# Kernel optimization log

Measured on AMD Instinct MI355X. Metric: run time of the kernel, lower is better.

Reference implementation:

```python
import jax, jax.numpy as jnp
import numpy as np

N, E, D, B, C = 50000, 800000, 128, 20000, 40
EPS_BN = 1e-3    # keras BatchNormalization default epsilon
EPS_NRM = 1e-12  # keras ops.nn.normalize epsilon
FFN_DIMS = {"pre": (D, D), "c1p": (D, D), "c1u": (2 * D, D), "c2p": (D, D), "c2u": (2 * D, D), "post": (D, D)}


def setup_inputs() -> dict:
    key = jax.random.key(0)
    ks = jax.random.split(key, 8)
    inp = {
        "node_features": jax.random.normal(ks[0], (N, D), jnp.float32),
        "edges": jax.random.randint(ks[1], (2, E), 0, N, dtype=jnp.int32),
        "edge_w": jax.random.uniform(ks[2], (E,), jnp.float32),
        "input_node_idx": jax.random.randint(ks[3], (B,), 0, N, dtype=jnp.int32),
    }
    for i, (name, (din, dout)) in enumerate(FFN_DIMS.items()):
        kw = jax.random.fold_in(key, 100 + i)
        inp[name + "_g"] = jnp.ones((din,), jnp.float32)
        inp[name + "_be"] = jnp.zeros((din,), jnp.float32)
        inp[name + "_mu"] = jnp.zeros((din,), jnp.float32)
        inp[name + "_var"] = jnp.ones((din,), jnp.float32)
        inp[name + "_w"] = jax.random.normal(kw, (din, dout), jnp.float32) * (1.0 / float(np.sqrt(din)))
        inp[name + "_bi"] = jnp.zeros((dout,), jnp.float32)
    inp["logits_w"] = jax.random.normal(ks[4], (D, C), jnp.float32) * (1.0 / float(np.sqrt(D)))
    inp["logits_b"] = jnp.zeros((C,), jnp.float32)
    return inp


def ffn(x, g, be, mu, var, w, bi):
    # BatchNorm (inference running stats) -> Dropout (identity) -> Dense + exact gelu
    xn = (x - mu) * jax.lax.rsqrt(var + EPS_BN) * g + be
    return jax.nn.gelu(xn @ w + bi, approximate=False)


def l2norm(x):
    n = jnp.sqrt(jnp.sum(x * x, axis=-1, keepdims=True))
    return x / jnp.maximum(n, EPS_NRM)


def graph_conv(x, node_idx, nbr_idx, ew, prep, upd):
    # gather neighbours -> prepare FFN -> edge-weighted -> segment_sum (reduce='sum')
    msgs = ffn(x[nbr_idx], *prep) * ew[:, None]                         # [E, D]
    red = jax.ops.segment_sum(msgs, node_idx, num_segments=x.shape[0])  # [N, D]
    h = jnp.concatenate([x, red], axis=1)                               # [N, 2D] (combination='concat')
    return l2norm(ffn(h, *upd))                                         # normalize=True


def reference(node_features, edges, edge_w, input_node_idx,
              pre_g, pre_be, pre_mu, pre_var, pre_w, pre_bi,
              c1p_g, c1p_be, c1p_mu, c1p_var, c1p_w, c1p_bi,
              c1u_g, c1u_be, c1u_mu, c1u_var, c1u_w, c1u_bi,
              c2p_g, c2p_be, c2p_mu, c2p_var, c2p_w, c2p_bi,
              c2u_g, c2u_be, c2u_mu, c2u_var, c2u_w, c2u_bi,
              post_g, post_be, post_mu, post_var, post_w, post_bi,
              logits_w, logits_b):
    ew = edge_w / jnp.sum(edge_w)                       # edge_W normalized at init
    node_idx, nbr_idx = edges[0], edges[1]
    x = ffn(node_features, pre_g, pre_be, pre_mu, pre_var, pre_w, pre_bi)
    x = graph_conv(x, node_idx, nbr_idx, ew,
                   (c1p_g, c1p_be, c1p_mu, c1p_var, c1p_w, c1p_bi),
                   (c1u_g, c1u_be, c1u_mu, c1u_var, c1u_w, c1u_bi)) + x
    x = graph_conv(x, node_idx, nbr_idx, ew,
                   (c2p_g, c2p_be, c2p_mu, c2p_var, c2p_w, c2p_bi),
                   (c2u_g, c2u_be, c2u_mu, c2u_var, c2u_w, c2u_bi)) + x
    x = ffn(x, post_g, post_be, post_mu, post_var, post_w, post_bi)
    return x[input_node_idx] @ logits_w + logits_b      # [B, C]
```

## Files before the change

kernel.cpp:

```cpp
#include <hip/hip_runtime.h>
#include <hip/hip_fp16.h>
#include <math.h>

static constexpr int D = 128;
static constexpr int CAP = 64;
static constexpr float EPS_BN = 1e-3f;

typedef short short8 __attribute__((ext_vector_type(8)));
typedef short short4v __attribute__((ext_vector_type(4)));
typedef float float4v __attribute__((ext_vector_type(4)));

__device__ __forceinline__ float gelu_exact(float x) {
    return 0.5f * x * (1.0f + erff(x * 0.70710678118654752f));
}

__device__ __forceinline__ void f32_to_hilo(float f, short& h, short& l) {
    unsigned u = __float_as_uint(f);
    h = (short)(u >> 16);
    float hf = __uint_as_float(u & 0xFFFF0000u);
    unsigned lu = __float_as_uint(f - hf);
    l = (short)(lu >> 16);
}

__device__ __forceinline__ short f32_to_bf16_rne(float f) {
    unsigned u = __float_as_uint(f);
    u += 0x7FFFu + ((u >> 16) & 1u);
    return (short)(u >> 16);
}

__device__ __forceinline__ void cvt_hilo8(const float4& x, const float4& y, short8& h8, short8& l8) {
    short h, l;
    f32_to_hilo(x.x, h, l); h8[0] = h; l8[0] = l;
    f32_to_hilo(x.y, h, l); h8[1] = h; l8[1] = l;
    f32_to_hilo(x.z, h, l); h8[2] = h; l8[2] = l;
    f32_to_hilo(x.w, h, l); h8[3] = h; l8[3] = l;
    f32_to_hilo(y.x, h, l); h8[4] = h; l8[4] = l;
    f32_to_hilo(y.y, h, l); h8[5] = h; l8[5] = l;
    f32_to_hilo(y.z, h, l); h8[6] = h; l8[6] = l;
    f32_to_hilo(y.w, h, l); h8[7] = h; l8[7] = l;
}

__device__ __forceinline__ short8 cvt_rne8(const float4& x, const float4& y) {
    short8 r;
    r[0] = f32_to_bf16_rne(x.x); r[1] = f32_to_bf16_rne(x.y);
    r[2] = f32_to_bf16_rne(x.z); r[3] = f32_to_bf16_rne(x.w);
    r[4] = f32_to_bf16_rne(y.x); r[5] = f32_to_bf16_rne(y.y);
    r[6] = f32_to_bf16_rne(y.z); r[7] = f32_to_bf16_rne(y.w);
    return r;
}

struct FoldArgs {
    const float* g[6]; const float* be[6]; const float* mu[6];
    const float* var[6]; const float* w[6]; const float* bi[6];
    short* wh[6]; short* wl[6]; float* bp[6]; int K[6];
};

__global__ void k_fold(FoldArgs fa) {
    __shared__ float sm[4];
    const int tid = threadIdx.x;
    const int lane = tid & 63, wvi = tid >> 6;
    const int f = blockIdx.x >> 7;
    const int c = blockIdx.x & 127;
    const int K = fa.K[f];
    const float* g = fa.g[f]; const float* be = fa.be[f];
    const float* mu = fa.mu[f]; const float* var = fa.var[f];
    const float* w = fa.w[f]; const float* bi = fa.bi[f];
    short* wh = fa.wh[f]; short* wl = fa.wl[f]; float* bp = fa.bp[f];
    float part = 0.f;
    for (int k = tid; k < K; k += blockDim.x) {
        float a = g[k] / sqrtf(var[k] + EPS_BN);
        float wv = w[k * D + c];
        float prod = a * wv;
        short hh, ll;
        f32_to_hilo(prod, hh, ll);
        wh[c * K + k] = hh;
        wl[c * K + k] = ll;
        part += (be[k] - mu[k] * a) * wv;
    }
    for (int off = 32; off > 0; off >>= 1) part += __shfl_down(part, off, 64);
    if (lane == 0) sm[wvi] = part;
    __syncthreads();
    if (tid == 0) bp[c] = bi[c] + sm[0] + sm[1] + sm[2] + sm[3];
}

__global__ void __launch_bounds__(512) k_fillpre(
    const int* __restrict__ edges, const float* __restrict__ ew,
    int* __restrict__ cnt, float* __restrict__ sums, unsigned* __restrict__ cw,
    int E, int N,
    const float* __restrict__ A0, const short* __restrict__ Wh,
    const short* __restrict__ Wl, const float* __restrict__ bp,
    float* __restrict__ outf,
    const short* __restrict__ Wh1, const float* __restrict__ bp1,
    __half* __restrict__ yh)
{
    constexpr int K = 128;
    constexpr int WSZ = 128 * K;
    __shared__ short Wlds[2 * WSZ];
    __shared__ short xbuf[2][16][136];
    __shared__ float sm[8];

    const int tid = threadIdx.x;
    const int lane = tid & 63;
    const int wvi = tid >> 6;

    if ((int)blockIdx.x < 256) {
        const int rid = blockIdx.x;
        const int g = rid & 7;
        const int bid = rid >> 3;
        const int gstride = 32 * 512;
        const int N8 = (N + 7) >> 3;
        const int lo = g * N8;
        const int hi = min(lo + N8, N);
        float s = 0.f;
        for (int e = bid * 512 + tid; e < E; e += gstride) {
            int dst = edges[e];
            if (dst >= lo && dst < hi) {
                int src = edges[E + e];
                float w = ew[e];
                s += w;
                unsigned short wb = __half_as_ushort(__float2half(w));
                int idx = atomicAdd(&cnt[dst], 1);
                if (idx < CAP)
                    cw[(size_t)dst * CAP + idx] = ((unsigned)src << 16) | (unsigned)wb;
            }
        }
        for (int off = 32; off > 0; off >>= 1) s += __shfl_down(s, off, 64);
        if (lane == 0) sm[wvi] = s;
        __syncthreads();
        if (tid == 0) {
            float t = 0.f;
            #pragma unroll
            for (int i = 0; i < 8; i++) t += sm[i];
            if (t != 0.f) atomicAdd(sums, t);
        }
        return;
    }

    const int fbid = blockIdx.x - 256;
    constexpr int NBLK = 768;

    #pragma unroll
    for (int it = 0; it < (2 * WSZ) / (512 * 8); ++it) {
        int s = it * 4096 + tid * 8;
        int buf = s / WSZ;
        int rem = s - buf * WSZ;
        int c = rem / K;
        int kk = (rem & (K - 1)) ^ ((c & 7) << 3);
        const short* src = (buf ? Wl : Wh) + c * K + kk;
        *(short8*)&Wlds[s] = *(const short8*)src;
    }
    __syncthreads();

    const int wv = tid >> 6;
    const int ssub = wv >> 2;
    const int wc = wv & 3;
    const int m = lane & 15;
    const int quad = lane >> 4;
    const int nstrips = (N + 15) >> 4;
    constexpr int STRIDE = NBLK * 2;

    int remw = nstrips - fbid * 2;
    int nit = remw > 0 ? (remw + STRIDE - 1) / STRIDE : 0;

    for (int it = 0; it < nit; ++it) {
        const int strip = fbid * 2 + ssub + it * STRIDE;
        const bool active = strip < nstrips;
        float4v acc[2];
        acc[0] = (float4v){0.f, 0.f, 0.f, 0.f};
        acc[1] = (float4v){0.f, 0.f, 0.f, 0.f};

        if (active) {
            int r = strip * 16 + m;
            if (r >= N) r = N - 1;
            const float* pA0 = A0 + (size_t)r * D;

            float4 a[2][4];
            {
                const float4* s4 = (const float4*)pA0 + quad * 2;
                a[0][0] = s4[0]; a[0][1] = s4[1]; a[0][2] = s4[8]; a[0][3] = s4[9];
            }
            {
                const float4* s4 = (const float4*)(pA0 + 64) + quad * 2;
                a[1][0] = s4[0]; a[1][1] = s4[1]; a[1][2] = s4[8]; a[1][3] = s4[9];
            }

            #pragma unroll
            for (int cc = 0; cc < 2; ++cc) {
                #pragma unroll
                for (int ks = 0; ks < 2; ++ks) {
                    const int kk = cc * 64 + ks * 32 + quad * 8;
                    short8 ah, al;
                    cvt_hilo8(a[cc][ks * 2], a[cc][ks * 2 + 1], ah, al);
                    #pragma unroll
                    for (int tj = 0; tj < 2; ++tj) {
                        const int c = wc * 32 + tj * 16 + m;
                        const int idx = c * K + (kk ^ ((c & 7) << 3));
                        short8 bh = *(const short8*)&Wlds[idx];
                        short8 bl = *(const short8*)&Wlds[WSZ + idx];
                        acc[tj] = __builtin_amdgcn_mfma_f32_16x16x32_bf16(al, bh, acc[tj], 0, 0, 0);
                        acc[tj] = __builtin_amdgcn_mfma_f32_16x16x32_bf16(ah, bl, acc[tj], 0, 0, 0);
                        acc[tj] = __builtin_amdgcn_mfma_f32_16x16x32_bf16(ah, bh, acc[tj], 0, 0, 0);
                    }
                }
            }

            #pragma unroll
            for (int tj = 0; tj < 2; ++tj) {
                float bv = bp[wc * 32 + tj * 16 + m];
                #pragma unroll
                for (int r4 = 0; r4 < 4; ++r4)
                    acc[tj][r4] = gelu_exact(acc[tj][r4] + bv);
            }
            #pragma unroll
            for (int r4 = 0; r4 < 4; ++r4) {
                int rib = quad * 4 + r4;
                int row = strip * 16 + rib;
                #pragma unroll
                for (int tj = 0; tj < 2; ++tj) {
                    int col = wc * 32 + tj * 16 + m;
                    if (row < N) outf[(size_t)row * D + col] = acc[tj][r4];
                    xbuf[ssub][rib][col] = f32_to_bf16_rne(acc[tj][r4]);
                }
            }
        }
        __syncthreads();

        if (active) {
            float4v acc2[2];
            acc2[0] = (float4v){0.f, 0.f, 0.f, 0.f};
            acc2[1] = (float4v){0.f, 0.f, 0.f, 0.f};
            #pragma unroll
            for (int cc = 0; cc < 2; ++cc) {
                #pragma unroll
                for (int ks = 0; ks < 2; ++ks) {
                    const int kk = cc * 64 + ks * 32 + quad * 8;
                    short8 ah = *(const short8*)&xbuf[ssub][m][kk];
                    #pragma unroll
                    for (int tj = 0; tj < 2; ++tj) {
                        const int c = wc * 32 + tj * 16 + m;
                        short8 bh = *(const short8*)(Wh1 + (size_t)c * 128 + kk);
                        acc2[tj] = __builtin_amdgcn_mfma_f32_16x16x32_bf16(ah, bh, acc2[tj], 0, 0, 0);
                    }
                }
            }
            #pragma unroll
            for (int tj = 0; tj < 2; ++tj) {
                float bv = bp1[wc * 32 + tj * 16 + m];
                #pragma unroll
                for (int r4 = 0; r4 < 4; ++r4)
                    acc2[tj][r4] = gelu_exact(acc2[tj][r4] + bv);
            }
            #pragma unroll
            for (int r4 = 0; r4 < 4; ++r4) {
                int row = strip * 16 + quad * 4 + r4;
                if (row < N) {
                    #pragma unroll
                    for (int tj = 0; tj < 2; ++tj) {
                        int col = wc * 32 + tj * 16 + m;
                        yh[(size_t)row * D + col] = __float2half(acc2[tj][r4]);
                    }
                }
            }
        }
        __syncthreads();
    }
}

__device__ __forceinline__ void accum8(float* acc, const float4& raw, float w) {
    const __half2* hp = (const __half2*)&raw;
    #pragma unroll
    for (int t = 0; t < 4; t++) {
        float2 f = __half22float2(hp[t]);
        acc[t * 2]     += w * f.x;
        acc[t * 2 + 1] += w * f.y;
    }
}

__global__ void k_reduce(const int* __restrict__ cnt, const unsigned* __restrict__ cw,
                         const float* __restrict__ sums, const __half* __restrict__ y,
                         float* __restrict__ red, int N) {
    int n = blockIdx.x * (blockDim.x >> 6) + (threadIdx.x >> 6);
    if (n >= N) return;
    float inv = 1.0f / sums[0];
    int lane = threadIdx.x & 63;
    int sub = lane >> 4;
    int q = lane & 15;
    int count = min(cnt[n], CAP);
    int start = n * CAP;
    int end = start + count;
    float acc[8] = {0.f, 0.f, 0.f, 0.f, 0.f, 0.f, 0.f, 0.f};
    int i = start + sub;
    for (; i + 12 < end; i += 16) {
        unsigned c0 = cw[i];
        unsigned c1 = cw[i + 4];
        unsigned c2 = cw[i + 8];
        unsigned c3 = cw[i + 12];
        float4 r0 = *((const float4*)(y + (size_t)(c0 >> 16) * D) + q);
        float4 r1 = *((const float4*)(y + (size_t)(c1 >> 16) * D) + q);
        float4 r2 = *((const float4*)(y + (size_t)(c2 >> 16) * D) + q);
        float4 r3 = *((const float4*)(y + (size_t)(c3 >> 16) * D) + q);
        float w0 = __half2float(__ushort_as_half((unsigned short)(c0 & 0xFFFFu))) * inv;
        float w1 = __half2float(__ushort_as_half((unsigned short)(c1 & 0xFFFFu))) * inv;
        float w2 = __half2float(__ushort_as_half((unsigned short)(c2 & 0xFFFFu))) * inv;
        float w3 = __half2float(__ushort_as_half((unsigned short)(c3 & 0xFFFFu))) * inv;
        accum8(acc, r0, w0);
        accum8(acc, r1, w1);
        accum8(acc, r2, w2);
        accum8(acc, r3, w3);
    }
    for (; i < end; i += 4) {
        unsigned c = cw[i];
        float4 r = *((const float4*)(y + (size_t)(c >> 16) * D) + q);
        float w = __half2float(__ushort_as_half((unsigned short)(c & 0xFFFFu))) * inv;
        accum8(acc, r, w);
    }
    #pragma unroll
    for (int t = 0; t < 8; t++) {
        acc[t] += __shfl_xor(acc[t], 16, 64);
        acc[t] += __shfl_xor(acc[t], 32, 64);
    }
    if (sub == 0) {
        float4 o0 = {acc[0], acc[1], acc[2], acc[3]};
        float4 o1 = {acc[4], acc[5], acc[6], acc[7]};
        *((float4*)(red + (size_t)n * D + q * 8)) = o0;
        *((float4*)(red + (size_t)n * D + q * 8 + 4)) = o1;
    }
}

template<int K, int BLOCK, bool SPLIT3, bool L2RES, bool OUT16, bool GATHER, bool FUSEP>
__global__ void __launch_bounds__(BLOCK, BLOCK / 256) k_ffn(
    const float* __restrict__ A0, const float* __restrict__ A1,
    const short* __restrict__ Wh, const short* __restrict__ Wl,
    const float* __restrict__ bp, const float* __restrict__ resid,
    float* __restrict__ outf, __half* __restrict__ outh, int N,
    const int* __restrict__ gidx,
    const short* __restrict__ WhP, const float* __restrict__ bpP,
    __half* __restrict__ yhP)
{
    constexpr int NB = SPLIT3 ? 2 : 1;
    constexpr int WSZ = 128 * K;
    constexpr int NC = K / 64;
    constexpr int SS = BLOCK / 256;
    __shared__ short Wlds[NB * WSZ];
    __shared__ float rsum[SS][16][4];
    __shared__ short xbuf[FUSEP ? SS : 1][16][136];

    const int tid = threadIdx.x;

    constexpr int ITER = (NB * WSZ) / (BLOCK * 8);
    #pragma unroll
    for (int it = 0; it < ITER; ++it) {
        int s = it * (BLOCK * 8) + tid * 8;
        int buf = s / WSZ;
        int rem = s - buf * WSZ;
        int c = rem / K;
        int kk = (rem & (K - 1)) ^ ((c & 7) << 3);
        const short* src = (buf ? Wl : Wh) + c * K + kk;
        *(short8*)&Wlds[s] = *(const short8*)src;
    }
    __syncthreads();

    const int lane = tid & 63;
    const int wv = tid >> 6;
    const int ssub = wv >> 2;
    const int wc = wv & 3;
    const int m = lane & 15;
    const int quad = lane >> 4;
    const int nstrips = (N + 15) >> 4;
    const int stride = gridDim.x * SS;
    const int base = blockIdx.x * SS + ssub;

    auto body = [&](int strip, bool active) {
        int rr = active ? strip * 16 + m : m;
        if (rr >= N) rr = N - 1;
        const int r = GATHER ? gidx[rr] : rr;
        const float* pA0 = A0 + (size_t)r * D;
        const float* pA1 = (K == 256) ? (A1 + (size_t)r * D) : pA0;

        float4 a[2][4];
        {
            const float4* s4 = (const float4*)pA0 + quad * 2;
            a[0][0] = s4[0]; a[0][1] = s4[1]; a[0][2] = s4[8]; a[0][3] = s4[9];
        }
        {
            const float4* s4 = (const float4*)(pA0 + 64) + quad * 2;
            a[1][0] = s4[0]; a[1][1] = s4[1]; a[1][2] = s4[8]; a[1][3] = s4[9];
        }

        float4v acc[2];
        acc[0] = (float4v){0.f, 0.f, 0.f, 0.f};
        acc[1] = (float4v){0.f, 0.f, 0.f, 0.f};

        #pragma unroll
        for (int cc = 0; cc < NC; ++cc) {
            #pragma unroll
            for (int ks = 0; ks < 2; ++ks) {
                const int kk = cc * 64 + ks * 32 + quad * 8;
                short8 ah, al;
                if (SPLIT3) cvt_hilo8(a[cc & 1][ks * 2], a[cc & 1][ks * 2 + 1], ah, al);
                else        ah = cvt_rne8(a[cc & 1][ks * 2], a[cc & 1][ks * 2 + 1]);
                #pragma unroll
                for (int tj = 0; tj < 2; ++tj) {
                    const int c = wc * 32 + tj * 16 + m;
                    const int idx = c * K + (kk ^ ((c & 7) << 3));
                    short8 bh = *(const short8*)&Wlds[idx];
                    if (SPLIT3) {
                        short8 bl = *(const short8*)&Wlds[WSZ + idx];
                        acc[tj] = __builtin_amdgcn_mfma_f32_16x16x32_bf16(al, bh, acc[tj], 0, 0, 0);
                        acc[tj] = __builtin_amdgcn_mfma_f32_16x16x32_bf16(ah, bl, acc[tj], 0, 0, 0);
                    }
                    acc[tj] = __builtin_amdgcn_mfma_f32_16x16x32_bf16(ah, bh, acc[tj], 0, 0, 0);
                }
            }
            if (cc + 2 < NC) {
                const int n2 = cc + 2;
                const float* src = (K == 256 && n2 >= 2) ? pA1 : pA0;
                const int kb = (K == 256) ? ((n2 & 1) * 64) : (n2 * 64);
                const float4* s4 = (const float4*)(src + kb) + quad * 2;
                a[cc & 1][0] = s4[0]; a[cc & 1][1] = s4[1];
                a[cc & 1][2] = s4[8]; a[cc & 1][3] = s4[9];
            }
        }

        #pragma unroll
        for (int tj = 0; tj < 2; ++tj) {
            float bv = bp[wc * 32 + tj * 16 + m];
            #pragma unroll
            for (int r4 = 0; r4 < 4; ++r4)
                acc[tj][r4] = gelu_exact(acc[tj][r4] + bv);
        }

        if (L2RES) {
            float ss[4];
            #pragma unroll
            for (int r4 = 0; r4 < 4; ++r4) {
                float v = acc[0][r4] * acc[0][r4] + acc[1][r4] * acc[1][r4];
                v += __shfl_xor(v, 1, 64);
                v += __shfl_xor(v, 2, 64);
                v += __shfl_xor(v, 4, 64);
                v += __shfl_xor(v, 8, 64);
                ss[r4] = v;
            }
            if (m == 0) {
                #pragma unroll
                for (int r4 = 0; r4 < 4; ++r4) rsum[ssub][quad * 4 + r4][wc] = ss[r4];
            }
            __syncthreads();
            #pragma unroll
            for (int r4 = 0; r4 < 4; ++r4) {
                const int rib = quad * 4 + r4;
                float tot = rsum[ssub][rib][0] + rsum[ssub][rib][1]
                          + rsum[ssub][rib][2] + rsum[ssub][rib][3];
                float inv = 1.0f / fmaxf(sqrtf(tot), 1e-12f);
                int row = strip * 16 + rib;
                if (active && row < N) {
                    #pragma unroll
                    for (int tj = 0; tj < 2; ++tj) {
                        int col = wc * 32 + tj * 16 + m;
                        float v = acc[tj][r4] * inv + resid[(size_t)row * D + col];
                        outf[(size_t)row * D + col] = v;
                        if (FUSEP) xbuf[ssub][rib][col] = f32_to_bf16_rne(v);
                    }
                }
            }
            if (FUSEP) {
                __syncthreads();
                if (active) {
                    float4v acc2[2];
                    acc2[0] = (float4v){0.f, 0.f, 0.f, 0.f};
                    acc2[1] = (float4v){0.f, 0.f, 0.f, 0.f};
                    #pragma unroll
                    for (int cc = 0; cc < 2; ++cc) {
                        #pragma unroll
                        for (int ks = 0; ks < 2; ++ks) {
                            const int kk = cc * 64 + ks * 32 + quad * 8;
                            short8 ah = *(const short8*)&xbuf[ssub][m][kk];
                            #pragma unroll
                            for (int tj = 0; tj < 2; ++tj) {
                                const int c = wc * 32 + tj * 16 + m;
                                short8 bh = *(const short8*)(WhP + (size_t)c * 128 + kk);
                                acc2[tj] = __builtin_amdgcn_mfma_f32_16x16x32_bf16(ah, bh, acc2[tj], 0, 0, 0);
                            }
                        }
                    }
                    #pragma unroll
                    for (int tj = 0; tj < 2; ++tj) {
                        float bv = bpP[wc * 32 + tj * 16 + m];
                        #pragma unroll
                        for (int r4 = 0; r4 < 4; ++r4)
                            acc2[tj][r4] = gelu_exact(acc2[tj][r4] + bv);
                    }
                    #pragma unroll
                    for (int r4 = 0; r4 < 4; ++r4) {
                        int row = strip * 16 + quad * 4 + r4;
                        if (row < N) {
                            #pragma unroll
                            for (int tj = 0; tj < 2; ++tj) {
                                int col = wc * 32 + tj * 16 + m;
                                yhP[(size_t)row * D + col] = __float2half(acc2[tj][r4]);
                            }
                        }
                    }
                }
            }
            __syncthreads();
        } else {
            #pragma unroll
            for (int r4 = 0; r4 < 4; ++r4) {
                int row = strip * 16 + quad * 4 + r4;
                if (active && row < N) {
                    #pragma unroll
                    for (int tj = 0; tj < 2; ++tj) {
                        int col = wc * 32 + tj * 16 + m;
                        if (OUT16) outh[(size_t)row * D + col] = __float2half(acc[tj][r4]);
                        else       outf[(size_t)row * D + col] = acc[tj][r4];
                    }
                }
            }
        }
    };

    if (L2RES) {
        int rem = nstrips - blockIdx.x * SS;
        int nit = rem > 0 ? (rem + stride - 1) / stride : 0;
        for (int it = 0; it < nit; ++it) {
            int strip = base + it * stride;
            body(strip, strip < nstrips);
        }
    } else {
        for (int strip = base; strip < nstrips; strip += stride)
            body(strip, true);
    }
}

__global__ void k_logits(const float* __restrict__ x,
                         const float* __restrict__ LW, const float* __restrict__ lb,
                         float* __restrict__ out, int B) {
    int wid = blockIdx.x * 4 + (threadIdx.x >> 6);
    int lane = threadIdx.x & 63;
    if (wid >= B) return;
    if (lane >= 40) return;
    float acc = lb[lane];
    const float4* xr = (const float4*)(x + (size_t)wid * D);
    #pragma unroll 4
    for (int k4 = 0; k4 < 32; k4++) {
        float4 xv = xr[k4];
        acc += xv.x * LW[(4 * k4 + 0) * 40 + lane];
        acc += xv.y * LW[(4 * k4 + 1) * 40 + lane];
        acc += xv.z * LW[(4 * k4 + 2) * 40 + lane];
        acc += xv.w * LW[(4 * k4 + 3) * 40 + lane];
    }
    out[(size_t)wid * 40 + lane] = acc;
}

extern "C" void kernel_launch(void* const* d_in, const int* in_sizes, int n_in,
                              void* d_out, int out_size, void* d_ws, size_t ws_size,
                              hipStream_t stream) {
    const float* node_features = (const float*)d_in[0];
    const int*   edges         = (const int*)d_in[1];
    const float* edge_w        = (const float*)d_in[2];
    const int*   input_idx     = (const int*)d_in[3];
    const int N = in_sizes[0] / D;
    const int E = in_sizes[2];
    const int B = in_sizes[3];

    const float* P[6][6];
    for (int f = 0; f < 6; f++)
        for (int q = 0; q < 6; q++)
            P[f][q] = (const float*)d_in[4 + f * 6 + q];
    const float* logits_w = (const float*)d_in[40];
    const float* logits_b = (const float*)d_in[41];

    float* ws = (float*)d_ws;
    size_t nd = (size_t)N * D;
    float* xA  = ws;
    float* y   = ws + nd;
    float* red = ws + 2 * nd;
    float* p   = ws + 3 * nd;
    __half* yh = (__half*)p; p += nd / 2;
    const int Ks[6] = {128, 128, 256, 128, 256, 128};
    short* Wh[6]; short* Wl[6]; float* Bp[6];
    {
        short* sp = (short*)p;
        for (int f = 0; f < 6; f++) {
            Wh[f] = sp; sp += (size_t)Ks[f] * D;
            Wl[f] = sp; sp += (size_t)Ks[f] * D;
        }
        p = (float*)sp;
    }
    for (int f = 0; f < 6; f++) { Bp[f] = p; p += D; }
    int* cnt    = (int*)p; p += N;
    float* sums = p; p += 2;
    unsigned* cw = (unsigned*)p; p += (size_t)N * CAP;

    FoldArgs fa;
    for (int f = 0; f < 6; f++) {
        fa.g[f] = P[f][0]; fa.be[f] = P[f][1]; fa.mu[f] = P[f][2];
        fa.var[f] = P[f][3]; fa.w[f] = P[f][4]; fa.bi[f] = P[f][5];
        fa.wh[f] = Wh[f]; fa.wl[f] = Wl[f]; fa.bp[f] = Bp[f]; fa.K[f] = Ks[f];
    }

    hipMemsetAsync(cnt, 0, ((size_t)N + 2) * sizeof(int), stream);
    k_fold<<<768, 256, 0, stream>>>(fa);
    k_fillpre<<<1024, 512, 0, stream>>>(edges, edge_w, cnt, sums, cw, E, N,
                                        node_features, Wh[0], Wl[0], Bp[0], xA,
                                        Wh[1], Bp[1], yh);

    const int rb = (N + 3) / 4;
    const int g1 = 256;
    const int g2 = 512;

    k_reduce<<<rb, 256, 0, stream>>>(cnt, cw, sums, yh, red, N);
    k_ffn<256, 1024, true,  true,  false, false, true ><<<g1, 1024, 0, stream>>>(
        xA, red, Wh[2], Wl[2], Bp[2], xA, y, nullptr, N, nullptr, Wh[3], Bp[3], yh);
    k_reduce<<<rb, 256, 0, stream>>>(cnt, cw, sums, yh, red, N);
    k_ffn<256, 1024, true,  true,  false, false, false><<<g1, 1024, 0, stream>>>(
        y, red, Wh[4], Wl[4], Bp[4], y, xA, nullptr, N, nullptr, nullptr, nullptr, nullptr);
    k_ffn<128, 512,  true,  false, false, true,  false><<<g2, 512, 0, stream>>>(
        xA, nullptr, Wh[5], Wl[5], Bp[5], nullptr, red, nullptr, B, input_idx, nullptr, nullptr, nullptr);
    k_logits<<<(B + 3) / 4, 256, 0, stream>>>(red, logits_w, logits_b, (float*)d_out, B);
}
```

Measured before the change: 438.2 us.

## Rebalance fused fill/pre-FFN kernel roles, unroll edge scan, hoist W1 fragments

Blocks of the fused CSR-fill and pre-FFN kernel are now assigned in interleaved groups of 256, and the split changes from 256 fill and 768 FFN blocks to 512 and 512, so the edge scan runs with twice the parallelism alongside the GEMM work. The edge loop is unrolled four-way so several loads are in flight before the atomics. The second-GEMM weight fragments are loaded into registers once per block instead of every strip, and launch bounds now ask for 4 blocks per SM. The trade-off is fewer FFN blocks and more register pressure.

```diff
diff --git a/kernel.cpp b/kernel.cpp
--- a/kernel.cpp
+++ b/kernel.cpp
@@ -83,7 +83,7 @@
     if (tid == 0) bp[c] = bi[c] + sm[0] + sm[1] + sm[2] + sm[3];
 }
 
-__global__ void __launch_bounds__(512) k_fillpre(
+__global__ void __launch_bounds__(512, 4) k_fillpre(
     const int* __restrict__ edges, const float* __restrict__ ew,
     int* __restrict__ cnt, float* __restrict__ sums, unsigned* __restrict__ cw,
     int E, int N,
@@ -103,25 +103,52 @@
     const int lane = tid & 63;
     const int wvi = tid >> 6;
 
-    if ((int)blockIdx.x < 256) {
-        const int rid = blockIdx.x;
+    const int grp = blockIdx.x >> 8;
+    const int role = grp & 1;
+    const int rid = ((grp >> 1) << 8) | (blockIdx.x & 255);
+
+    if (role == 0) {
         const int g = rid & 7;
         const int bid = rid >> 3;
-        const int gstride = 32 * 512;
+        const int gs = 64 * 512;
         const int N8 = (N + 7) >> 3;
         const int lo = g * N8;
         const int hi = min(lo + N8, N);
         float s = 0.f;
-        for (int e = bid * 512 + tid; e < E; e += gstride) {
-            int dst = edges[e];
-            if (dst >= lo && dst < hi) {
+        int e = bid * 512 + tid;
+        for (; e + 3 * gs < E; e += 4 * gs) {
+            int d0 = edges[e];
+            int d1 = edges[e + gs];
+            int d2 = edges[e + 2 * gs];
+            int d3 = edges[e + 3 * gs];
+            bool i0 = (d0 >= lo && d0 < hi);
+            bool i1 = (d1 >= lo && d1 < hi);
+            bool i2 = (d2 >= lo && d2 < hi);
+            bool i3 = (d3 >= lo && d3 < hi);
+            int s0 = 0, s1 = 0, s2 = 0, s3 = 0;
+            float w0 = 0.f, w1 = 0.f, w2 = 0.f, w3 = 0.f;
+            if (i0) { s0 = edges[E + e];          w0 = ew[e]; }
+            if (i1) { s1 = edges[E + e + gs];     w1 = ew[e + gs]; }
+            if (i2) { s2 = edges[E + e + 2 * gs]; w2 = ew[e + 2 * gs]; }
+            if (i3) { s3 = edges[E + e + 3 * gs]; w3 = ew[e + 3 * gs]; }
+            if (i0) { s += w0; int x = atomicAdd(&cnt[d0], 1);
+                if (x < CAP) cw[(size_t)d0 * CAP + x] = ((unsigned)s0 << 16) | (unsigned)__half_as_ushort(__float2half(w0)); }
+            if (i1) { s += w1; int x = atomicAdd(&cnt[d1], 1);
+                if (x < CAP) cw[(size_t)d1 * CAP + x] = ((unsigned)s1 << 16) | (unsigned)__half_as_ushort(__float2half(w1)); }
+            if (i2) { s += w2; int x = atomicAdd(&cnt[d2], 1);
+                if (x < CAP) cw[(size_t)d2 * CAP + x] = ((unsigned)s2 << 16) | (unsigned)__half_as_ushort(__float2half(w2)); }
+            if (i3) { s += w3; int x = atomicAdd(&cnt[d3], 1);
+                if (x < CAP) cw[(size_t)d3 * CAP + x] = ((unsigned)s3 << 16) | (unsigned)__half_as_ushort(__float2half(w3)); }
+        }
+        for (; e < E; e += gs) {
+            int d = edges[e];
+            if (d >= lo && d < hi) {
                 int src = edges[E + e];
                 float w = ew[e];
                 s += w;
-                unsigned short wb = __half_as_ushort(__float2half(w));
-                int idx = atomicAdd(&cnt[dst], 1);
-                if (idx < CAP)
-                    cw[(size_t)dst * CAP + idx] = ((unsigned)src << 16) | (unsigned)wb;
+                int x = atomicAdd(&cnt[d], 1);
+                if (x < CAP)
+                    cw[(size_t)d * CAP + x] = ((unsigned)src << 16) | (unsigned)__half_as_ushort(__float2half(w));
             }
         }
         for (int off = 32; off > 0; off >>= 1) s += __shfl_down(s, off, 64);
@@ -136,8 +163,8 @@
         return;
     }
 
-    const int fbid = blockIdx.x - 256;
-    constexpr int NBLK = 768;
+    const int fbid = rid;
+    constexpr int NBLK = 512;
 
     #pragma unroll
     for (int it = 0; it < (2 * WSZ) / (512 * 8); ++it) {
@@ -159,6 +186,18 @@
     const int nstrips = (N + 15) >> 4;
     constexpr int STRIDE = NBLK * 2;
 
+    short8 w1f[2][2][2];
+    #pragma unroll
+    for (int cc = 0; cc < 2; ++cc)
+        #pragma unroll
+        for (int ks = 0; ks < 2; ++ks)
+            #pragma unroll
+            for (int tj = 0; tj < 2; ++tj) {
+                const int kk = cc * 64 + ks * 32 + quad * 8;
+                const int c = wc * 32 + tj * 16 + m;
+                w1f[cc][ks][tj] = *(const short8*)(Wh1 + (size_t)c * 128 + kk);
+            }
+
     int remw = nstrips - fbid * 2;
     int nit = remw > 0 ? (remw + STRIDE - 1) / STRIDE : 0;
 
@@ -236,11 +275,8 @@
                     const int kk = cc * 64 + ks * 32 + quad * 8;
                     short8 ah = *(const short8*)&xbuf[ssub][m][kk];
                     #pragma unroll
-                    for (int tj = 0; tj < 2; ++tj) {
-                        const int c = wc * 32 + tj * 16 + m;
-                        short8 bh = *(const short8*)(Wh1 + (size_t)c * 128 + kk);
-                        acc2[tj] = __builtin_amdgcn_mfma_f32_16x16x32_bf16(ah, bh, acc2[tj], 0, 0, 0);
-                    }
+                    for (int tj = 0; tj < 2; ++tj)
+                        acc2[tj] = __builtin_amdgcn_mfma_f32_16x16x32_bf16(ah, w1f[cc][ks][tj], acc2[tj], 0, 0, 0);
                 }
             }
             #pragma unroll
```

Result: no change. 434.7 us (-0.8%).
